# Performance work log

Hardware: AMD Instinct MI355X
Metric: run time of the kernel (lower is better)

## Reference

```python
import jax, jax.numpy as jnp
import numpy as np
from math import sqrt, log

N_PATCHES = 128
ATTN_WINDOW = 10
NEG_INF = -10000.0


def _causal_mask(L):
    # patch id per position; query patch i may attend key patch j iff 0 < (j_pid - i_pid) < window
    channels = L // N_PATCHES
    pid = jnp.repeat(jnp.arange(N_PATCHES), channels)  # [L]
    diff = pid[None, :] - pid[:, None]                 # [L_query, L_key] = pid[key]-pid[query]
    return (diff <= 0) | (diff >= ATTN_WINDOW)         # True => blocked


def setup_inputs() -> dict:
    key = jax.random.key(0)
    kq, kk, kv = jax.random.split(key, 3)
    B, H, L, D = 4, 8, 1024, 64
    return {
        "queries": jax.random.normal(kq, (B, H, L, D), dtype=jnp.float32),
        "keys": jax.random.normal(kk, (B, H, L, D), dtype=jnp.float32),
        "values": jax.random.normal(kv, (B, H, L, D), dtype=jnp.float32),
        "log_scale": jnp.asarray(np.log(2.0), dtype=jnp.float32),
    }


def reference(queries, keys, values, log_scale):
    B, H, L, D = queries.shape
    scores = jnp.einsum("bhld,bhmd->bhlm", queries, keys)           # [B,H,L,L]
    scale = jnp.clip(jnp.exp(log_scale), 1.0, 30.0) / sqrt(D)
    mask = _causal_mask(L)                                          # [L,L]
    pos = jnp.where(mask, NEG_INF, scores)
    neg = jnp.where(mask, NEG_INF, -scores)
    A = jax.nn.softmax(scale * pos, axis=-1) - jax.nn.softmax(scale * neg, axis=-1)
    V = jnp.einsum("bhlm,bhmd->bhld", A, values)
    return V
```

## Files before the change

kernel.cpp:

```cpp
#include <hip/hip_runtime.h>
#include <math.h>

#define NPATCH 128
#define CH 8
#define D 64
#define WIN 9
#define G 4
#define NKEY 96
#define STR 97

typedef _Float16 h2 __attribute__((ext_vector_type(2)));

static __device__ __forceinline__ h2 pkrtz(float x, float y) {
    return __builtin_bit_cast(h2, __builtin_amdgcn_cvt_pkrtz(x, y));
}
static __device__ __forceinline__ unsigned h2u(h2 h) { return __builtin_bit_cast(unsigned, h); }
static __device__ __forceinline__ h2 u2h(unsigned u) { return __builtin_bit_cast(h2, u); }

__global__ __launch_bounds__(256) void signed_attn_kernel(
    const float* __restrict__ Q, const float* __restrict__ K,
    const float* __restrict__ V, const float* __restrict__ logscale,
    float* __restrict__ O)
{
    __shared__ unsigned sK[8 * STR * 4];
    __shared__ unsigned sV[8 * STR * 4];
    __shared__ unsigned sA[G * CH * 72];

    const int tid = threadIdx.x;
    const int grp = blockIdx.x & 31;
    const int bh  = blockIdx.x >> 5;
    const int p0  = grp * G;

    const long long base = (long long)bh * (NPATCH * CH) * D;
    const int nst = min(NKEY, (NPATCH - 1 - p0) * CH);

    const float scale = fminf(fmaxf(__expf(logscale[0]), 1.0f), 30.0f) * 0.125f;

    {
        const long long kb = base + (long long)((p0 + 1) * CH) * D;
        const float4* Kg = (const float4*)(K + kb);
        const float4* Vg = (const float4*)(V + kb);
        for (int i = tid; i < nst * 16; i += 256) {
            const int k = i >> 4, d4 = i & 15, c = d4 >> 1, hh = d4 & 1;
            const float4 kv = Kg[i];
            const float4 vv = Vg[i];
            const int dst = (c * STR + k) * 4 + hh * 2;
            *(uint2*)&sK[dst] = make_uint2(h2u(pkrtz(kv.x, kv.y)), h2u(pkrtz(kv.z, kv.w)));
            *(uint2*)&sV[dst] = make_uint2(h2u(pkrtz(vv.x, vv.y)), h2u(pkrtz(vv.z, vv.w)));
        }
        for (int i = tid; i < (NKEY - nst) * 8; i += 256) {
            const int k = nst + (i >> 3), c = i & 7;
            *(uint4*)&sV[(c * STR + k) * 4] = make_uint4(0u, 0u, 0u, 0u);
        }
    }
    __syncthreads();

    const int q     = tid >> 3;
    const int lane8 = tid & 7;
    const int g     = q >> 3;
    const int p     = p0 + g;
    const int krel0 = g * CH;
    const int kvmax = min(72, (NPATCH - 1 - p) * CH);

    const float4* Qrow = (const float4*)(Q + base + (long long)(p * CH + (q & 7)) * D);

    h2 acc[9];
#pragma unroll
    for (int j = 0; j < 9; ++j) acc[j] = 0;

#pragma unroll 2
    for (int c = 0; c < 8; ++c) {
        const float4 q0 = Qrow[2 * c];
        const float4 q1 = Qrow[2 * c + 1];
        const h2 qh0 = pkrtz(q0.x, q0.y), qh1 = pkrtz(q0.z, q0.w);
        const h2 qh2 = pkrtz(q1.x, q1.y), qh3 = pkrtz(q1.z, q1.w);
        const unsigned* kc = &sK[c * STR * 4];
#pragma unroll
        for (int j = 0; j < 9; ++j) {
            const uint4 kv = *(const uint4*)&kc[(krel0 + lane8 + 8 * j) * 4];
            acc[j] += qh0 * u2h(kv.x) + qh1 * u2h(kv.y) + qh2 * u2h(kv.z) + qh3 * u2h(kv.w);
        }
    }

    float t[9];
    bool  vld[9];
#pragma unroll
    for (int j = 0; j < 9; ++j) {
        t[j]   = scale * ((float)acc[j][0] + (float)acc[j][1]);
        vld[j] = (lane8 + 8 * j) < kvmax;
    }

    float mp = -1e30f, mn = -1e30f;
#pragma unroll
    for (int j = 0; j < 9; ++j) {
        mp = fmaxf(mp, vld[j] ?  t[j] : -1e30f);
        mn = fmaxf(mn, vld[j] ? -t[j] : -1e30f);
    }
#pragma unroll
    for (int off = 4; off > 0; off >>= 1) {
        mp = fmaxf(mp, __shfl_xor(mp, off));
        mn = fmaxf(mn, __shfl_xor(mn, off));
    }

    float ep[9], en[9], sp = 0.f, sn = 0.f;
#pragma unroll
    for (int j = 0; j < 9; ++j) {
        ep[j] = vld[j] ? __expf( t[j] - mp) : 0.f;
        en[j] = vld[j] ? __expf(-t[j] - mn) : 0.f;
        sp += ep[j]; sn += en[j];
    }
#pragma unroll
    for (int off = 4; off > 0; off >>= 1) {
        sp += __shfl_xor(sp, off);
        sn += __shfl_xor(sn, off);
    }
    const float rp = (sp > 0.f) ? 1.f / sp : 0.f;
    const float rn = (sn > 0.f) ? 1.f / sn : 0.f;

#pragma unroll
    for (int j = 0; j < 9; ++j) {
        const float A = ep[j] * rp - en[j] * rn;
        sA[q * 72 + lane8 + 8 * j] = h2u(pkrtz(A, A));
    }
    __syncthreads();

    const int c = tid & 7;
    h2 o0 = 0, o1 = 0, o2 = 0, o3 = 0;
    const unsigned* vc   = &sV[c * STR * 4];
    const unsigned* arow = &sA[q * 72];
#pragma unroll 8
    for (int kk = 0; kk < 72; ++kk) {
        const h2 av = u2h(arow[kk]);
        const uint4 vv = *(const uint4*)&vc[(krel0 + kk) * 4];
        o0 += u2h(vv.x) * av;
        o1 += u2h(vv.y) * av;
        o2 += u2h(vv.z) * av;
        o3 += u2h(vv.w) * av;
    }
    float4* Og4 = (float4*)(O + base + (long long)(p * CH + (q & 7)) * D + c * 8);
    Og4[0] = make_float4((float)o0[0], (float)o0[1], (float)o1[0], (float)o1[1]);
    Og4[1] = make_float4((float)o2[0], (float)o2[1], (float)o3[0], (float)o3[1]);
}

extern "C" void kernel_launch(void* const* d_in, const int* in_sizes, int n_in,
                              void* d_out, int out_size, void* d_ws, size_t ws_size,
                              hipStream_t stream) {
    const float* Q  = (const float*)d_in[0];
    const float* K  = (const float*)d_in[1];
    const float* V  = (const float*)d_in[2];
    const float* ls = (const float*)d_in[3];
    float* O = (float*)d_out;

    const int L = 1024;
    const int nBH = in_sizes[0] / (L * D);
    dim3 grid(nBH * (NPATCH / G));
    signed_attn_kernel<<<grid, 256, 0, stream>>>(Q, K, V, ls, O);
}
```

Before: 88.15 us.

## Compute banded QK^T and PV with MFMA 16x16x32 fp16 tiles

Replaces the packed-half scalar dot products with MFMA matrix instructions for both score and output matmuls. Each block now covers 8 patches (64 queries), stages Q, K and a transposed V in fp16 shared memory, and computes a dense 64x128 score tile that is then masked to the band. This raises the useful work rate and accumulates in fp32. In exchange it does redundant work on masked entries, halves the grid size, and uses more LDS per block.

```diff
diff --git a/kernel.cpp b/kernel.cpp
--- a/kernel.cpp
+++ b/kernel.cpp
@@ -4,31 +4,38 @@
 #define NPATCH 128
 #define CH 8
 #define D 64
-#define WIN 9
-#define G 4
-#define NKEY 96
-#define STR 97
+#define G 8
+#define NQ (G*CH)
+#define NKEY 128
+#define QSTR 72
+#define KSTR 72
+#define VSTR 136
+#define PSTR 136
 
-typedef _Float16 h2 __attribute__((ext_vector_type(2)));
+typedef __fp16 half8 __attribute__((ext_vector_type(8)));
+typedef float  f32x4 __attribute__((ext_vector_type(4)));
+typedef unsigned u32x4 __attribute__((ext_vector_type(4)));
 
-static __device__ __forceinline__ h2 pkrtz(float x, float y) {
-    return __builtin_bit_cast(h2, __builtin_amdgcn_cvt_pkrtz(x, y));
+static __device__ __forceinline__ unsigned pk(float x, float y) {
+    return __builtin_bit_cast(unsigned, __builtin_amdgcn_cvt_pkrtz(x, y));
 }
-static __device__ __forceinline__ unsigned h2u(h2 h) { return __builtin_bit_cast(unsigned, h); }
-static __device__ __forceinline__ h2 u2h(unsigned u) { return __builtin_bit_cast(h2, u); }
+static __device__ __forceinline__ half8 ld8(const unsigned short* p) {
+    return __builtin_bit_cast(half8, *(const u32x4*)p);
+}
 
 __global__ __launch_bounds__(256) void signed_attn_kernel(
     const float* __restrict__ Q, const float* __restrict__ K,
     const float* __restrict__ V, const float* __restrict__ logscale,
     float* __restrict__ O)
 {
-    __shared__ unsigned sK[8 * STR * 4];
-    __shared__ unsigned sV[8 * STR * 4];
-    __shared__ unsigned sA[G * CH * 72];
+    __shared__ __align__(16) unsigned short sQ[NQ * QSTR];
+    __shared__ __align__(16) unsigned short sK[NKEY * KSTR];
+    __shared__ __align__(16) unsigned short sVt[D * VSTR];
+    __shared__ __align__(16) unsigned short sP[NQ * PSTR];
 
     const int tid = threadIdx.x;
-    const int grp = blockIdx.x & 31;
-    const int bh  = blockIdx.x >> 5;
+    const int grp = blockIdx.x & 15;
+    const int bh  = blockIdx.x >> 4;
     const int p0  = grp * G;
 
     const long long base = (long long)bh * (NPATCH * CH) * D;
@@ -36,110 +43,112 @@
 
     const float scale = fminf(fmaxf(__expf(logscale[0]), 1.0f), 30.0f) * 0.125f;
 
-    {
-        const long long kb = base + (long long)((p0 + 1) * CH) * D;
-        const float4* Kg = (const float4*)(K + kb);
-        const float4* Vg = (const float4*)(V + kb);
-        for (int i = tid; i < nst * 16; i += 256) {
-            const int k = i >> 4, d4 = i & 15, c = d4 >> 1, hh = d4 & 1;
-            const float4 kv = Kg[i];
-            const float4 vv = Vg[i];
-            const int dst = (c * STR + k) * 4 + hh * 2;
-            *(uint2*)&sK[dst] = make_uint2(h2u(pkrtz(kv.x, kv.y)), h2u(pkrtz(kv.z, kv.w)));
-            *(uint2*)&sV[dst] = make_uint2(h2u(pkrtz(vv.x, vv.y)), h2u(pkrtz(vv.z, vv.w)));
-        }
-        for (int i = tid; i < (NKEY - nst) * 8; i += 256) {
-            const int k = nst + (i >> 3), c = i & 7;
-            *(uint4*)&sV[(c * STR + k) * 4] = make_uint4(0u, 0u, 0u, 0u);
-        }
+    const float4* Qg = (const float4*)(Q + base + (long long)(p0 * CH) * D);
+    for (int i = tid; i < NQ * 16; i += 256) {
+        const int row = i >> 4, d4 = i & 15;
+        const float4 v = Qg[i];
+        *(uint2*)&sQ[row * QSTR + d4 * 4] = make_uint2(pk(v.x, v.y), pk(v.z, v.w));
+    }
+    const float4* Kg = (const float4*)(K + base + (long long)((p0 + 1) * CH) * D);
+    for (int i = tid; i < NKEY * 16; i += 256) {
+        const int row = i >> 4, d4 = i & 15;
+        uint2 w = make_uint2(0u, 0u);
+        if (row < nst) { const float4 v = Kg[i]; w = make_uint2(pk(v.x, v.y), pk(v.z, v.w)); }
+        *(uint2*)&sK[row * KSTR + d4 * 4] = w;
+    }
+    const float4* Vg = (const float4*)(V + base + (long long)((p0 + 1) * CH) * D);
+    for (int u = tid; u < 64 * 16; u += 256) {
+        const int kp = u & 63, dq = u >> 6;
+        float4 va = make_float4(0.f, 0.f, 0.f, 0.f);
+        float4 vb = va;
+        if (2 * kp < nst) { va = Vg[(2 * kp) * 16 + dq]; vb = Vg[(2 * kp + 1) * 16 + dq]; }
+        *(unsigned*)&sVt[(dq * 4 + 0) * VSTR + 2 * kp] = pk(va.x, vb.x);
+        *(unsigned*)&sVt[(dq * 4 + 1) * VSTR + 2 * kp] = pk(va.y, vb.y);
+        *(unsigned*)&sVt[(dq * 4 + 2) * VSTR + 2 * kp] = pk(va.z, vb.z);
+        *(unsigned*)&sVt[(dq * 4 + 3) * VSTR + 2 * kp] = pk(va.w, vb.w);
     }
     __syncthreads();
 
-    const int q     = tid >> 3;
-    const int lane8 = tid & 7;
-    const int g     = q >> 3;
-    const int p     = p0 + g;
-    const int krel0 = g * CH;
-    const int kvmax = min(72, (NPATCH - 1 - p) * CH);
+    const int wav = tid >> 6, lane = tid & 63;
+    const int col = lane & 15, quad = lane >> 4;
 
-    const float4* Qrow = (const float4*)(Q + base + (long long)(p * CH + (q & 7)) * D);
+    const half8 a0 = ld8(&sQ[(wav * 16 + col) * QSTR + quad * 8]);
+    const half8 a1 = ld8(&sQ[(wav * 16 + col) * QSTR + 32 + quad * 8]);
 
-    h2 acc[9];
+    f32x4 acc[8];
 #pragma unroll
-    for (int j = 0; j < 9; ++j) acc[j] = 0;
+    for (int t = 0; t < 8; ++t) acc[t] = (f32x4){0.f, 0.f, 0.f, 0.f};
+#pragma unroll
+    for (int t = 0; t < 8; ++t) {
+        const half8 b0 = ld8(&sK[(t * 16 + col) * KSTR + quad * 8]);
+        const half8 b1 = ld8(&sK[(t * 16 + col) * KSTR + 32 + quad * 8]);
+        acc[t] = __builtin_amdgcn_mfma_f32_16x16x32_f16(a0, b0, acc[t], 0, 0, 0);
+        acc[t] = __builtin_amdgcn_mfma_f32_16x16x32_f16(a1, b1, acc[t], 0, 0, 0);
+    }
 
-#pragma unroll 2
-    for (int c = 0; c < 8; ++c) {
-        const float4 q0 = Qrow[2 * c];
-        const float4 q1 = Qrow[2 * c + 1];
-        const h2 qh0 = pkrtz(q0.x, q0.y), qh1 = pkrtz(q0.z, q0.w);
-        const h2 qh2 = pkrtz(q1.x, q1.y), qh3 = pkrtz(q1.z, q1.w);
-        const unsigned* kc = &sK[c * STR * 4];
 #pragma unroll
-        for (int j = 0; j < 9; ++j) {
-            const uint4 kv = *(const uint4*)&kc[(krel0 + lane8 + 8 * j) * 4];
-            acc[j] += qh0 * u2h(kv.x) + qh1 * u2h(kv.y) + qh2 * u2h(kv.z) + qh3 * u2h(kv.w);
+    for (int r = 0; r < 4; ++r) {
+        const int q   = wav * 16 + quad * 4 + r;
+        const int kr0 = (q >> 3) * 8;
+        const int kmx = min(kr0 + 72, nst);
+
+        float tv[8]; bool vl[8];
+        float mp = -1e30f, mn = -1e30f;
+#pragma unroll
+        for (int t = 0; t < 8; ++t) {
+            const int c = col + 16 * t;
+            tv[t] = scale * acc[t][r];
+            vl[t] = (c >= kr0) && (c < kmx);
+            mp = fmaxf(mp, vl[t] ?  tv[t] : -1e30f);
+            mn = fmaxf(mn, vl[t] ? -tv[t] : -1e30f);
+        }
+#pragma unroll
+        for (int off = 1; off < 16; off <<= 1) {
+            mp = fmaxf(mp, __shfl_xor(mp, off));
+            mn = fmaxf(mn, __shfl_xor(mn, off));
+        }
+        float ep[8], en[8], sp = 0.f, sn = 0.f;
+#pragma unroll
+        for (int t = 0; t < 8; ++t) {
+            ep[t] = vl[t] ? __expf( tv[t] - mp) : 0.f;
+            en[t] = vl[t] ? __expf(-tv[t] - mn) : 0.f;
+            sp += ep[t]; sn += en[t];
+        }
+#pragma unroll
+        for (int off = 1; off < 16; off <<= 1) {
+            sp += __shfl_xor(sp, off);
+            sn += __shfl_xor(sn, off);
+        }
+        const float rp = (sp > 0.f) ? 1.f / sp : 0.f;
+        const float rn = (sn > 0.f) ? 1.f / sn : 0.f;
+#pragma unroll
+        for (int t = 0; t < 8; ++t) {
+            const float A = ep[t] * rp - en[t] * rn;
+            sP[q * PSTR + col + 16 * t] = (unsigned short)pk(A, A);
         }
     }
 
-    float t[9];
-    bool  vld[9];
+    f32x4 oc[4];
 #pragma unroll
-    for (int j = 0; j < 9; ++j) {
-        t[j]   = scale * ((float)acc[j][0] + (float)acc[j][1]);
-        vld[j] = (lane8 + 8 * j) < kvmax;
+    for (int t = 0; t < 4; ++t) oc[t] = (f32x4){0.f, 0.f, 0.f, 0.f};
+#pragma unroll
+    for (int kq = 0; kq < 4; ++kq) {
+        const half8 ap = ld8(&sP[(wav * 16 + col) * PSTR + kq * 32 + quad * 8]);
+#pragma unroll
+        for (int t = 0; t < 4; ++t) {
+            const half8 bv = ld8(&sVt[(t * 16 + col) * VSTR + kq * 32 + quad * 8]);
+            oc[t] = __builtin_amdgcn_mfma_f32_16x16x32_f16(ap, bv, oc[t], 0, 0, 0);
+        }
     }
 
-    float mp = -1e30f, mn = -1e30f;
+    float* Ob = O + base + (long long)(p0 * CH) * D;
 #pragma unroll
-    for (int j = 0; j < 9; ++j) {
-        mp = fmaxf(mp, vld[j] ?  t[j] : -1e30f);
-        mn = fmaxf(mn, vld[j] ? -t[j] : -1e30f);
+    for (int t = 0; t < 4; ++t) {
+#pragma unroll
+        for (int r = 0; r < 4; ++r) {
+            Ob[(wav * 16 + quad * 4 + r) * D + t * 16 + col] = oc[t][r];
+        }
     }
-#pragma unroll
-    for (int off = 4; off > 0; off >>= 1) {
-        mp = fmaxf(mp, __shfl_xor(mp, off));
-        mn = fmaxf(mn, __shfl_xor(mn, off));
-    }
-
-    float ep[9], en[9], sp = 0.f, sn = 0.f;
-#pragma unroll
-    for (int j = 0; j < 9; ++j) {
-        ep[j] = vld[j] ? __expf( t[j] - mp) : 0.f;
-        en[j] = vld[j] ? __expf(-t[j] - mn) : 0.f;
-        sp += ep[j]; sn += en[j];
-    }
-#pragma unroll
-    for (int off = 4; off > 0; off >>= 1) {
-        sp += __shfl_xor(sp, off);
-        sn += __shfl_xor(sn, off);
-    }
-    const float rp = (sp > 0.f) ? 1.f / sp : 0.f;
-    const float rn = (sn > 0.f) ? 1.f / sn : 0.f;
-
-#pragma unroll
-    for (int j = 0; j < 9; ++j) {
-        const float A = ep[j] * rp - en[j] * rn;
-        sA[q * 72 + lane8 + 8 * j] = h2u(pkrtz(A, A));
-    }
-    __syncthreads();
-
-    const int c = tid & 7;
-    h2 o0 = 0, o1 = 0, o2 = 0, o3 = 0;
-    const unsigned* vc   = &sV[c * STR * 4];
-    const unsigned* arow = &sA[q * 72];
-#pragma unroll 8
-    for (int kk = 0; kk < 72; ++kk) {
-        const h2 av = u2h(arow[kk]);
-        const uint4 vv = *(const uint4*)&vc[(krel0 + kk) * 4];
-        o0 += u2h(vv.x) * av;
-        o1 += u2h(vv.y) * av;
-        o2 += u2h(vv.z) * av;
-        o3 += u2h(vv.w) * av;
-    }
-    float4* Og4 = (float4*)(O + base + (long long)(p * CH + (q & 7)) * D + c * 8);
-    Og4[0] = make_float4((float)o0[0], (float)o0[1], (float)o1[0], (float)o1[1]);
-    Og4[1] = make_float4((float)o2[0], (float)o2[1], (float)o3[0], (float)o3[1]);
 }
 
 extern "C" void kernel_launch(void* const* d_in, const int* in_sizes, int n_in,
```

Result: faster. 83.48 us (-5.3%).
